# Kernel optimization log

Hardware: AMD Instinct MI355X
Metric: run time of the kernel (lower is better)

## Reference

```python
import jax, jax.numpy as jnp
import numpy as np

IN_F = 512
OUT_F = 512
ALPHA = 0.2  # LeakyReLU negative slope
# dropout p=0.1 is a no-op at inference (training=False), so omitted


def setup_inputs() -> dict:
    key = jax.random.key(0)
    k1, k2, k3 = jax.random.split(key, 3)
    B, N = 16, 1024
    x = jax.random.normal(k1, (B, N, IN_F), dtype=jnp.float32)
    # xavier_uniform with gain=1.414
    limW = 1.414 * np.sqrt(6.0 / (IN_F + OUT_F))
    W = jax.random.uniform(k2, (IN_F, OUT_F), minval=-limW, maxval=limW, dtype=jnp.float32)
    lima = 1.414 * np.sqrt(6.0 / (2 * OUT_F + 1))
    a = jax.random.uniform(k3, (2 * OUT_F, 1), minval=-lima, maxval=lima, dtype=jnp.float32)
    beta = jnp.ones((1,), dtype=jnp.float32)
    return {"x": x, "W": W, "a": a, "beta": beta}


def reference(x, W, a, beta):
    # h: [B, N, F]
    h = jnp.matmul(x, W)
    # Split attention vector: e_ij = leakyrelu(h_i . a1 + h_j . a2)
    a1 = a[:OUT_F, 0]   # [F]
    a2 = a[OUT_F:, 0]   # [F]
    s1 = jnp.einsum('bnf,f->bn', h, a1)  # [B, N]
    s2 = jnp.einsum('bnf,f->bn', h, a2)  # [B, N]
    e = s1[:, :, None] + s2[:, None, :]  # [B, N, N]
    e = jnp.where(e > 0, e, ALPHA * e)   # LeakyReLU
    attention = jax.nn.softmax(e, axis=2)
    h_prime = jnp.einsum('bnm,bmf->bnf', attention, h)
    out = jax.nn.elu(h_prime + beta * h)
    return out
```

## Files before the change

kernel.cpp:

```cpp
#include <hip/hip_runtime.h>

using u16 = unsigned short;
using u32 = unsigned int;
using u64 = unsigned long long;

#define ALPHA 0.2f
#define LOG2E 1.4426950408889634f

typedef __bf16 bf16x8 __attribute__((ext_vector_type(8)));
typedef float f32x4 __attribute__((ext_vector_type(4)));
typedef float f32x16 __attribute__((ext_vector_type(16)));

__device__ __forceinline__ u16 f2bf(float f) {
  u32 u = __builtin_bit_cast(u32, f);
  u += 0x7FFFu + ((u >> 16) & 1u);
  return (u16)(u >> 16);
}
__device__ __forceinline__ float bf2f(u16 h) {
  u32 u = ((u32)h) << 16;
  return __builtin_bit_cast(float, u);
}
__device__ __forceinline__ void gload_lds16(const void* g, void* l) {
  __builtin_amdgcn_global_load_lds((__attribute__((address_space(1))) void*)g,
                                   (__attribute__((address_space(3))) void*)l,
                                   16, 0, 0);
}

__global__ __launch_bounds__(256) void k_cast_wT(const float* __restrict__ W, u16* __restrict__ wbt) {
  int idx = blockIdx.x * 256 + threadIdx.x;
  int k = idx >> 9, n = idx & 511;
  wbt[n * 512 + k] = f2bf(W[idx]);
}

__global__ __launch_bounds__(256, 2) void k_gemm1(const float* __restrict__ x, const u16* __restrict__ wbt,
                                                  const float* __restrict__ a,
                                                  u16* __restrict__ hbf,
                                                  float* __restrict__ s1p, float* __restrict__ s2p) {
  __shared__ __attribute__((aligned(16))) char lds[73728];
  __shared__ __attribute__((aligned(16))) float a_l[256];

  const int t = threadIdx.x;
  const int lane = t & 63;
  const int w = t >> 6;
  const int l31 = lane & 31, lhi = lane >> 5;
  const int rb = w >> 1, cg = w & 1;
  const int g = blockIdx.x;
  const int cb = (g >> 3) & 3;
  const int tile_m = (g & 7) | ((g >> 5) << 3);
  const int row0 = tile_m * 128;
  const int col0 = cb * 128;

  a_l[t] = (t < 128) ? a[col0 + t] : a[512 + col0 + (t - 128)];

  f32x16 acc[2][2];
#pragma unroll
  for (int i = 0; i < 2; ++i)
#pragma unroll
    for (int j = 0; j < 2; ++j)
#pragma unroll
      for (int r = 0; r < 16; ++r) acc[i][j][r] = 0.f;

#define STAGE_G1(kt, Ab, Bb)                                                              \
  {                                                                                       \
    const int k0_ = (kt) * 32;                                                            \
    _Pragma("unroll")                                                                     \
    for (int i = 0; i < 4; ++i) {                                                         \
      int G = i * 256 + t;                                                                \
      int row = G >> 3, ks = G & 7;                                                       \
      gload_lds16(x + (size_t)(row0 + row) * 512 + k0_ + ((ks ^ (row & 7)) * 4),          \
                  (Ab) + (size_t)(i * 256 + w * 64) * 16);                                \
    }                                                                                     \
    _Pragma("unroll")                                                                     \
    for (int i = 0; i < 2; ++i) {                                                         \
      int G = i * 256 + t;                                                                \
      int col = G >> 2, ks = G & 3;                                                       \
      gload_lds16(wbt + (size_t)(col0 + col) * 512 + k0_ + ((ks ^ ((col >> 1) & 3)) * 8), \
                  (Bb) + (size_t)(i * 256 + w * 64) * 16);                                \
    }                                                                                     \
  }

#define COMPUTE_G1(Ab, Bb)                                                                         \
  {                                                                                                \
    _Pragma("unroll")                                                                              \
    for (int ks = 0; ks < 2; ++ks) {                                                               \
      bf16x8 af[2];                                                                                \
      _Pragma("unroll")                                                                            \
      for (int sub = 0; sub < 2; ++sub) {                                                          \
        const int arow = rb * 64 + sub * 32 + l31;                                                 \
        const int kg = ks * 4 + lhi * 2;                                                           \
        f32x4 fa0 = *reinterpret_cast<const f32x4*>((Ab) + (size_t)(arow * 8 + (kg ^ (arow & 7))) * 16); \
        f32x4 fa1 = *reinterpret_cast<const f32x4*>((Ab) + (size_t)(arow * 8 + ((kg + 1) ^ (arow & 7))) * 16); \
        _Pragma("unroll")                                                                          \
        for (int jj = 0; jj < 4; ++jj) {                                                           \
          af[sub][jj] = (__bf16)fa0[jj];                                                           \
          af[sub][jj + 4] = (__bf16)fa1[jj];                                                       \
        }                                                                                          \
      }                                                                                            \
      bf16x8 bfr[2];                                                                               \
      _Pragma("unroll")                                                                            \
      for (int bt = 0; bt < 2; ++bt) {                                                             \
        const int bcol = cg * 64 + bt * 32 + l31;                                                  \
        const int kslot = (ks * 2 + lhi) ^ ((bcol >> 1) & 3);                                      \
        bfr[bt] = *reinterpret_cast<const bf16x8*>((Bb) + (size_t)(bcol * 4 + kslot) * 16);        \
      }                                                                                            \
      _Pragma("unroll")                                                                            \
      for (int sub = 0; sub < 2; ++sub)                                                            \
        _Pragma("unroll")                                                                          \
        for (int bt = 0; bt < 2; ++bt)                                                             \
          acc[sub][bt] = __builtin_amdgcn_mfma_f32_32x32x16_bf16(af[sub], bfr[bt], acc[sub][bt], 0, 0, 0); \
    }                                                                                              \
  }

  char* Ac = lds;             char* Bc = lds + 49152;
  char* An = lds + 16384;     char* Bn = lds + 57344;
  char* As = lds + 32768;     char* Bs = lds + 65536;

  STAGE_G1(0, Ac, Bc);
  STAGE_G1(1, An, Bn);
  __builtin_amdgcn_sched_barrier(0);
  asm volatile("s_waitcnt vmcnt(6) lgkmcnt(0)" ::: "memory");
  __builtin_amdgcn_s_barrier();
  __builtin_amdgcn_sched_barrier(0);

#pragma unroll 1
  for (int kt = 0; kt < 14; ++kt) {
    STAGE_G1(kt + 2, As, Bs);
    COMPUTE_G1(Ac, Bc);
    __builtin_amdgcn_sched_barrier(0);
    asm volatile("s_waitcnt vmcnt(6)" ::: "memory");
    __builtin_amdgcn_s_barrier();
    __builtin_amdgcn_sched_barrier(0);
    char* ta = Ac; Ac = An; An = As; As = ta;
    char* tb = Bc; Bc = Bn; Bn = Bs; Bs = tb;
  }
  COMPUTE_G1(Ac, Bc);
  __builtin_amdgcn_sched_barrier(0);
  asm volatile("s_waitcnt vmcnt(0)" ::: "memory");
  __builtin_amdgcn_s_barrier();
  __builtin_amdgcn_sched_barrier(0);
  COMPUTE_G1(An, Bn);
#undef STAGE_G1
#undef COMPUTE_G1

  __syncthreads();

  u16* lT = (u16*)lds;
#pragma unroll
  for (int sub = 0; sub < 2; ++sub)
#pragma unroll
    for (int bt = 0; bt < 2; ++bt) {
      const int col = cg * 64 + bt * 32 + l31;
#pragma unroll
      for (int r = 0; r < 16; ++r) {
        int row = rb * 64 + sub * 32 + (r & 3) + 8 * (r >> 2) + 4 * lhi;
        lT[row * 136 + col] = f2bf(acc[sub][bt][r]);
      }
    }
  __syncthreads();

#pragma unroll
  for (int i = 0; i < 8; ++i) {
    int G = i * 256 + t;
    int row = G >> 4, gg = G & 15;
    uint4 v = *reinterpret_cast<const uint4*>(&lT[row * 136 + gg * 8]);
    *reinterpret_cast<uint4*>(&hbf[(size_t)(row0 + row) * 512 + col0 + gg * 8]) = v;
  }
  {
    const int r2 = t >> 1, half = t & 1;
    float d1 = 0.f, d2 = 0.f;
#pragma unroll
    for (int i = 0; i < 8; ++i) {
      uint4 v = *reinterpret_cast<const uint4*>(&lT[r2 * 136 + half * 64 + i * 8]);
      u32 wds[4] = {v.x, v.y, v.z, v.w};
#pragma unroll
      for (int jj = 0; jj < 8; ++jj) {
        float h = bf2f((u16)(wds[jj >> 1] >> ((jj & 1) * 16)));
        d1 += h * a_l[half * 64 + i * 8 + jj];
        d2 += h * a_l[128 + half * 64 + i * 8 + jj];
      }
    }
    d1 += __shfl_xor(d1, 1);
    d2 += __shfl_xor(d2, 1);
    if (half == 0) {
      s1p[cb * 16384 + row0 + r2] = d1;
      s2p[cb * 16384 + row0 + r2] = d2;
    }
  }
}

__global__ __launch_bounds__(1024) void k_prep(const float* __restrict__ s1p, const float* __restrict__ s2p,
                                               float* __restrict__ e1s, float* __restrict__ e2s,
                                               u32* __restrict__ permM, u32* __restrict__ kng,
                                               float* __restrict__ c1ig, float* __restrict__ c2ig) {
  __shared__ u32 sk[1024];
  __shared__ float s2all[1024];
  __shared__ float s2sv[1024];
  __shared__ float arrA[1024];
  __shared__ float arrB[1024];
  const int b = blockIdx.x;
  const int t = threadIdx.x;
  const int id = b * 1024 + t;

  const float s1v = (s1p[id] + s1p[16384 + id] + s1p[32768 + id] + s1p[49152 + id]) * LOG2E;
  const float s2v = (s2p[id] + s2p[16384 + id] + s2p[32768 + id] + s2p[49152 + id]) * LOG2E;
  s2all[t] = s2v;

  {
    u32 bits = __builtin_bit_cast(u32, s2v);
    u32 key = (bits & 0x80000000u) ? ~bits : (bits | 0x80000000u);
    sk[t] = (key & 0xFFFFFC00u) | (u32)t;
  }
  for (int size = 2; size <= 1024; size <<= 1)
    for (int stride = size >> 1; stride > 0; stride >>= 1) {
      __syncthreads();
      int ixj = t ^ stride;
      if (ixj > t) {
        u32 va = sk[t], vb = sk[ixj];
        bool asc = ((t & size) == 0);
        if ((va > vb) == asc) { sk[t] = vb; sk[ixj] = va; }
      }
    }
  __syncthreads();

  const u32 idx = sk[t] & 1023u;
  const float sv = s2all[idx];
  s2sv[t] = sv;
  __syncthreads();

  const float E1 = exp2f(sv), E2 = exp2f(ALPHA * sv);
  e1s[b * 1024 + t] = E1;
  e2s[b * 1024 + t] = E2;
  permM[b * 1024 + t] = idx;
  arrA[t] = E2;
  arrB[t] = exp2f(s2sv[1023 - t]);
  __syncthreads();

  for (int off = 1; off < 1024; off <<= 1) {
    float aA = (t >= off) ? arrA[t - off] : 0.f;
    float aB = (t >= off) ? arrB[t - off] : 0.f;
    __syncthreads();
    arrA[t] += aA;
    arrB[t] += aB;
    __syncthreads();
  }

  {
    const float thr = -s1v;
    int lo = 0, hi = 1024;
    while (lo < hi) { int mid = (lo + hi) >> 1; if (s2sv[mid] <= thr) lo = mid + 1; else hi = mid; }
    const int kn = lo;
    float se1suf = (kn == 1024) ? 0.f : arrB[1023 - kn];
    float se2pre = (kn == 0) ? 0.f : arrA[kn - 1];
    const float c1 = exp2f(s1v), c2 = exp2f(ALPHA * s1v);
    const float inv = 1.0f / (c1 * se1suf + c2 * se2pre);
    c1ig[id] = c1 * inv;
    c2ig[id] = c2 * inv;
    kng[id] = (u32)kn;
  }
}

__global__ __launch_bounds__(256, 2) void k_sweep2(const u16* __restrict__ hbf,
                                                   const float* __restrict__ e1s, const float* __restrict__ e2s,
                                                   const u32* __restrict__ permM, const u32* __restrict__ kng,
                                                   const float* __restrict__ c1ig, const float* __restrict__ c2ig,
                                                   const float* __restrict__ betag, float* __restrict__ out) {
  __shared__ u32 Cp[257][16];
  __shared__ float e1_l[1024];
  __shared__ float e2_l[1024];
  __shared__ float c1i_l[1024];
  __shared__ float c2i_l[1024];
  __shared__ u16 kn_l[1024];
  __shared__ u16 perm_l[1024];
  __shared__ float segS1[16][16];
  __shared__ float segP2[16][16];

  const int t = threadIdx.x;
  const int B = blockIdx.x;
  const int b = (B & 7) * 2 + ((B >> 3) & 1);
  const int fc = B >> 4;

  const u16* hB = hbf + (size_t)b * 1024 * 512 + fc * 16;

#pragma unroll
  for (int q = 0; q < 4; ++q) {
    int i = q * 256 + t;
    e1_l[i] = e1s[b * 1024 + i];
    e2_l[i] = e2s[b * 1024 + i];
    c1i_l[i] = c1ig[b * 1024 + i];
    c2i_l[i] = c2ig[b * 1024 + i];
    kn_l[i] = (u16)kng[b * 1024 + i];
    perm_l[i] = (u16)permM[b * 1024 + i];
  }
  __syncthreads();

  const int f = t & 15;
  const int seg = t >> 4;
  float ch1[16], ch2[16];
  float ss1 = 0.f, ss2 = 0.f;
#pragma unroll
  for (int c = 0; c < 16; ++c) {
    const int i0 = seg * 64 + c * 4;
    float a1 = 0.f, a2 = 0.f;
#pragma unroll
    for (int ii = 0; ii < 4; ++ii) {
      const int i = i0 + ii;
      float hv = bf2f(hB[(size_t)perm_l[i] * 512 + f]);
      a1 = fmaf(e1_l[i], hv, a1);
      a2 = fmaf(e2_l[i], hv, a2);
    }
    ch1[c] = a1; ch2[c] = a2;
    ss1 += a1; ss2 += a2;
  }
  segS1[seg][f] = ss1;
  segP2[seg][f] = ss2;
  __syncthreads();

  float sufAfter = 0.f, preBefore = 0.f, totP2 = 0.f;
#pragma unroll
  for (int s7 = 0; s7 < 16; ++s7) {
    float v1 = segS1[s7][f];
    float v2 = segP2[s7][f];
    if (s7 > seg) sufAfter += v1;
    if (s7 < seg) preBefore += v2;
    totP2 += v2;
  }
  {
    float run1 = sufAfter;
    float c1v[16];
#pragma unroll
    for (int c = 15; c >= 0; --c) { run1 += ch1[c]; c1v[c] = run1; }
    float run2 = preBefore;
#pragma unroll
    for (int c = 0; c < 16; ++c) {
      Cp[seg * 16 + c][f] = (u32)f2bf(c1v[c]) | ((u32)f2bf(run2) << 16);
      run2 += ch2[c];
    }
  }
  if (seg == 0) Cp[256][f] = (u32)f2bf(0.f) | ((u32)f2bf(totP2) << 16);
  __syncthreads();

  const float beta = betag[0];
  const int nl = t >> 4;
#pragma unroll 4
  for (int r = 0; r < 64; ++r) {
    const int n = r * 16 + nl;
    const int kn = kn_l[n];
    const int cn = kn >> 2;
    const int rn = kn & 3;
    const int i0 = cn * 4;
    float p1 = 0.f, p2 = 0.f;
#pragma unroll
    for (int ii = 0; ii < 3; ++ii) {
      int idx = i0 + ii;
      idx = idx > 1023 ? 1023 : idx;
      float hv = bf2f(hB[(size_t)perm_l[idx] * 512 + f]);
      float w1 = (ii < rn) ? e1_l[idx] : 0.f;
      float w2 = (ii < rn) ? e2_l[idx] : 0.f;
      p1 = fmaf(w1, hv, p1);
      p2 = fmaf(w2, hv, p2);
    }
    const u32 cp = Cp[cn][f];
    const float A = bf2f((u16)(cp & 0xFFFFu)) - p1;
    const float Bv = bf2f((u16)(cp >> 16)) + p2;
    const float hvn = bf2f(hB[(size_t)n * 512 + f]);
    const float xv = c1i_l[n] * A + c2i_l[n] * Bv + beta * hvn;
    out[((size_t)b * 1024 + n) * 512 + fc * 16 + f] = xv > 0.f ? xv : __expf(xv) - 1.0f;
  }
}

extern "C" void kernel_launch(void* const* d_in, const int* in_sizes, int n_in,
                              void* d_out, int out_size, void* d_ws, size_t ws_size,
                              hipStream_t stream) {
  const float* x = (const float*)d_in[0];
  const float* W = (const float*)d_in[1];
  const float* a = (const float*)d_in[2];
  const float* beta = (const float*)d_in[3];
  float* out = (float*)d_out;

  char* ws = (char*)d_ws;
  u16* hbf = (u16*)ws;
  char* sm = ws + (16u << 20);
  float* e1s = (float*)(sm);
  float* e2s = (float*)(sm + (64u << 10));
  u32* permM = (u32*)(sm + (128u << 10));
  u32* kng = (u32*)(sm + (192u << 10));
  float* c1i = (float*)(sm + (256u << 10));
  float* c2i = (float*)(sm + (320u << 10));
  float* s1p = (float*)(sm + (512u << 10));
  float* s2p = (float*)(sm + (768u << 10));
  u16* wbt = (u16*)(sm + (1024u << 10));

  k_cast_wT<<<1024, 256, 0, stream>>>(W, wbt);
  k_gemm1<<<512, 256, 0, stream>>>(x, wbt, a, hbf, s1p, s2p);
  k_prep<<<16, 1024, 0, stream>>>(s1p, s2p, e1s, e2s, permM, kng, c1i, c2i);
  k_sweep2<<<512, 256, 0, stream>>>(hbf, e1s, e2s, permM, kng, c1i, c2i, beta, out);
}
```

Measured before the change: 74.38 us.

## Store full-resolution prefix/suffix sums in LDS to drop per-row correction gathers

After: 66.64 us. 1.12x faster.

```diff
diff --git a/kernel.cpp b/kernel.cpp
--- a/kernel.cpp
+++ b/kernel.cpp
@@ -264,13 +264,11 @@
                                                    const u32* __restrict__ permM, const u32* __restrict__ kng,
                                                    const float* __restrict__ c1ig, const float* __restrict__ c2ig,
                                                    const float* __restrict__ betag, float* __restrict__ out) {
-  __shared__ u32 Cp[257][16];
-  __shared__ float e1_l[1024];
-  __shared__ float e2_l[1024];
+  __shared__ u16 Cp1[1025][16];
+  __shared__ u16 Cp2[1025][16];
   __shared__ float c1i_l[1024];
   __shared__ float c2i_l[1024];
   __shared__ u16 kn_l[1024];
-  __shared__ u16 perm_l[1024];
   __shared__ float segS1[16][16];
   __shared__ float segP2[16][16];
 
@@ -284,59 +282,61 @@
 #pragma unroll
   for (int q = 0; q < 4; ++q) {
     int i = q * 256 + t;
-    e1_l[i] = e1s[b * 1024 + i];
-    e2_l[i] = e2s[b * 1024 + i];
     c1i_l[i] = c1ig[b * 1024 + i];
     c2i_l[i] = c2ig[b * 1024 + i];
     kn_l[i] = (u16)kng[b * 1024 + i];
-    perm_l[i] = (u16)permM[b * 1024 + i];
-  }
-  __syncthreads();
+  }
 
   const int f = t & 15;
   const int seg = t >> 4;
-  float ch1[16], ch2[16];
+  const int i0 = seg * 64;
+  const u32* permB = permM + b * 1024 + i0;
+  const float* e1B = e1s + b * 1024 + i0;
+  const float* e2B = e2s + b * 1024 + i0;
+
+  u32 hpk[32];
   float ss1 = 0.f, ss2 = 0.f;
-#pragma unroll
-  for (int c = 0; c < 16; ++c) {
-    const int i0 = seg * 64 + c * 4;
-    float a1 = 0.f, a2 = 0.f;
-#pragma unroll
-    for (int ii = 0; ii < 4; ++ii) {
-      const int i = i0 + ii;
-      float hv = bf2f(hB[(size_t)perm_l[i] * 512 + f]);
-      a1 = fmaf(e1_l[i], hv, a1);
-      a2 = fmaf(e2_l[i], hv, a2);
-    }
-    ch1[c] = a1; ch2[c] = a2;
-    ss1 += a1; ss2 += a2;
+#pragma unroll 8
+  for (int c = 0; c < 64; c += 2) {
+    u16 h0 = hB[(size_t)permB[c] * 512 + f];
+    u16 h1 = hB[(size_t)permB[c + 1] * 512 + f];
+    hpk[c >> 1] = (u32)h0 | ((u32)h1 << 16);
+    ss1 = fmaf(e1B[c], bf2f(h0), ss1);
+    ss1 = fmaf(e1B[c + 1], bf2f(h1), ss1);
+    ss2 = fmaf(e2B[c], bf2f(h0), ss2);
+    ss2 = fmaf(e2B[c + 1], bf2f(h1), ss2);
   }
   segS1[seg][f] = ss1;
   segP2[seg][f] = ss2;
   __syncthreads();
 
-  float sufAfter = 0.f, preBefore = 0.f, totP2 = 0.f;
+  float sufAfter = 0.f, preBefore = 0.f;
 #pragma unroll
   for (int s7 = 0; s7 < 16; ++s7) {
-    float v1 = segS1[s7][f];
-    float v2 = segP2[s7][f];
-    if (s7 > seg) sufAfter += v1;
-    if (s7 < seg) preBefore += v2;
-    totP2 += v2;
-  }
+    if (s7 > seg) sufAfter += segS1[s7][f];
+    if (s7 < seg) preBefore += segP2[s7][f];
+  }
+
+  if (seg == 15) Cp1[1024][f] = 0;
   {
     float run1 = sufAfter;
-    float c1v[16];
-#pragma unroll
-    for (int c = 15; c >= 0; --c) { run1 += ch1[c]; c1v[c] = run1; }
+#pragma unroll
+    for (int c = 63; c >= 0; --c) {
+      u16 hv = (u16)((hpk[c >> 1] >> ((c & 1) * 16)) & 0xFFFFu);
+      run1 = fmaf(e1B[c], bf2f(hv), run1);
+      Cp1[i0 + c][f] = f2bf(run1);
+    }
+  }
+  {
     float run2 = preBefore;
 #pragma unroll
-    for (int c = 0; c < 16; ++c) {
-      Cp[seg * 16 + c][f] = (u32)f2bf(c1v[c]) | ((u32)f2bf(run2) << 16);
-      run2 += ch2[c];
-    }
-  }
-  if (seg == 0) Cp[256][f] = (u32)f2bf(0.f) | ((u32)f2bf(totP2) << 16);
+    for (int c = 0; c < 64; ++c) {
+      Cp2[i0 + c][f] = f2bf(run2);
+      u16 hv = (u16)((hpk[c >> 1] >> ((c & 1) * 16)) & 0xFFFFu);
+      run2 = fmaf(e2B[c], bf2f(hv), run2);
+    }
+    if (seg == 15) Cp2[1024][f] = f2bf(run2);
+  }
   __syncthreads();
 
   const float beta = betag[0];
@@ -345,23 +345,8 @@
   for (int r = 0; r < 64; ++r) {
     const int n = r * 16 + nl;
     const int kn = kn_l[n];
-    const int cn = kn >> 2;
-    const int rn = kn & 3;
-    const int i0 = cn * 4;
-    float p1 = 0.f, p2 = 0.f;
-#pragma unroll
-    for (int ii = 0; ii < 3; ++ii) {
-      int idx = i0 + ii;
-      idx = idx > 1023 ? 1023 : idx;
-      float hv = bf2f(hB[(size_t)perm_l[idx] * 512 + f]);
-      float w1 = (ii < rn) ? e1_l[idx] : 0.f;
-      float w2 = (ii < rn) ? e2_l[idx] : 0.f;
-      p1 = fmaf(w1, hv, p1);
-      p2 = fmaf(w2, hv, p2);
-    }
-    const u32 cp = Cp[cn][f];
-    const float A = bf2f((u16)(cp & 0xFFFFu)) - p1;
-    const float Bv = bf2f((u16)(cp >> 16)) + p2;
+    const float A = bf2f(Cp1[kn][f]);
+    const float Bv = bf2f(Cp2[kn][f]);
     const float hvn = bf2f(hB[(size_t)n * 512 + f]);
     const float xv = c1i_l[n] * A + c2i_l[n] * Bv + beta * hvn;
     out[((size_t)b * 1024 + n) * 512 + fc * 16 + f] = xv > 0.f ? xv : __expf(xv) - 1.0f;
```
